# Kernel tuning notes

Measured on AMD Instinct MI355X. Metric: run time of the kernel, lower is better.

The kernel has to match this reference:

```python
import jax, jax.numpy as jnp
import numpy as np

FILTER_SIZE = 1024
NUM_HEADS = 16
D_HEAD = FILTER_SIZE // NUM_HEADS
LN_EPS = 1e-5


def setup_inputs() -> dict:
    key = jax.random.key(0)
    ks = jax.random.split(key, 10)
    B, T, D = 2, 2048, FILTER_SIZE
    s = 1.0 / np.sqrt(D)
    return {
        "x": jax.random.normal(ks[0], (B, T, D), dtype=jnp.float32),
        "Wq": jax.random.normal(ks[1], (D, D), dtype=jnp.float32) * s,
        "bq": jnp.zeros((D,), dtype=jnp.float32),
        "Wk": jax.random.normal(ks[2], (D, D), dtype=jnp.float32) * s,
        "bk": jnp.zeros((D,), dtype=jnp.float32),
        "Wv": jax.random.normal(ks[3], (D, D), dtype=jnp.float32) * s,
        "bv": jnp.zeros((D,), dtype=jnp.float32),
        "Wo": jax.random.normal(ks[4], (D, D), dtype=jnp.float32) * s,
        "bo": jnp.zeros((D,), dtype=jnp.float32),
        "gamma": jnp.ones((D,), dtype=jnp.float32),
        "beta": jnp.zeros((D,), dtype=jnp.float32),
    }


def reference(x, Wq, bq, Wk, bk, Wv, bv, Wo, bo, gamma, beta):
    B, T, D = x.shape
    H, Dh = NUM_HEADS, D_HEAD
    # Note: source splits features as (d_head, heads) with heads LAST.
    q = (x @ Wq.T + bq).reshape(B, T, Dh, H)
    k = (x @ Wk.T + bk).reshape(B, T, Dh, H)
    v = (x @ Wv.T + bv).reshape(B, T, Dh, H)
    scale = 1.0 / np.sqrt(Dh).astype(np.float32)
    # scores: (B, H, T, T)
    scores = jnp.einsum("bidh,bjdh->bhij", q, k) * scale
    attn = jax.nn.softmax(scores, axis=-1)  # dropout is identity in eval
    out = jnp.einsum("bhij,bjdh->bidh", attn, v)  # (B, T, Dh, H)
    out = out.reshape(B, T, D)  # matches permute(0,2,3,1).reshape in torch
    out = out @ Wo.T + bo
    out = out + x
    mu = jnp.mean(out, axis=-1, keepdims=True)
    var = jnp.var(out, axis=-1, keepdims=True)
    out = (out - mu) * jax.lax.rsqrt(var + LN_EPS) * gamma + beta
    return out
```

## Files before the change

### kernel.cpp

```cpp
#include <hip/hip_runtime.h>
#include <stdint.h>

#define T_SEQ 2048
#define D_MODEL 1024
#define NH 16
#define DH 64
#define NROWS 4096

typedef __bf16 bf16x8 __attribute__((ext_vector_type(8)));
typedef float floatx4 __attribute__((ext_vector_type(4)));
typedef short short4v __attribute__((ext_vector_type(4)));
typedef short short8v __attribute__((ext_vector_type(8)));

#define AS1 __attribute__((address_space(1)))
#define AS3 __attribute__((address_space(3)))

static __device__ __forceinline__ void gl2lds16(const unsigned short* g, unsigned short* s) {
    __builtin_amdgcn_global_load_lds((const AS1 unsigned int*)g, (AS3 unsigned int*)s, 16, 0, 0);
}

static __device__ __forceinline__ unsigned short f32_bf16(float f) {
    union { float f; unsigned int u; } c; c.f = f;
    unsigned int u = c.u;
    u = u + 0x7FFFu + ((u >> 16) & 1u);
    return (unsigned short)(u >> 16);
}

static __device__ __forceinline__ unsigned int pack2_bf16(float a, float b) {
    return (unsigned int)f32_bf16(a) | ((unsigned int)f32_bf16(b) << 16);
}

static __device__ __forceinline__ floatx4 mfma16(bf16x8 a, bf16x8 b, floatx4 c) {
    return __builtin_amdgcn_mfma_f32_16x16x32_bf16(a, b, c, 0, 0, 0);
}

static __device__ __forceinline__ floatx4 mfma16k16(short4v a, short4v b, floatx4 c) {
#if defined(__HIP_DEVICE_COMPILE__)
    return __builtin_amdgcn_mfma_f32_16x16x16bf16_1k(a, b, c, 0, 0, 0);
#else
    (void)a; (void)b;
    return c;
#endif
}

#define QSCALE 0.1803368801111204f
#define EXP2_SHIFT 10.0f
#define WAITCNT_VM(n) (0x0F70 | (n))

__global__ __launch_bounds__(256) void k_conv_all(const float* __restrict__ x,
                                                  const float* __restrict__ Wq,
                                                  const float* __restrict__ Wk,
                                                  const float* __restrict__ Wv,
                                                  const float* __restrict__ Wo,
                                                  unsigned short* __restrict__ x_bf,
                                                  unsigned short* __restrict__ wqkv_bf,
                                                  unsigned short* __restrict__ wo_bf) {
    int b = blockIdx.x, t = threadIdx.x;
    if (b < 4096) {
        int i = b * 1024 + t * 4;
        float4 v = *(const float4*)(x + i);
        uint2 o;
        o.x = pack2_bf16(v.x, v.y);
        o.y = pack2_bf16(v.z, v.w);
        *(uint2*)(x_bf + i) = o;
    } else if (b < 7168) {
        int idx = b - 4096;
        int tensor = idx >> 10, np = idx & 1023;
        const float* src = tensor == 0 ? Wq : tensor == 1 ? Wk : Wv;
        int f = (np & 63) * 16 + (np >> 6);
        int c = t * 4;
        float4 v = *(const float4*)(src + (long)f * D_MODEL + c);
        uint2 o;
        o.x = pack2_bf16(v.x, v.y);
        o.y = pack2_bf16(v.z, v.w);
        *(uint2*)(wqkv_bf + ((long)tensor * D_MODEL + np) * D_MODEL + c) = o;
    } else {
        int n = b - 7168;
        int fp = t * 4;
        const float* row = Wo + (long)n * D_MODEL;
        unsigned short o[4];
        #pragma unroll
        for (int k = 0; k < 4; k++) {
            int f = fp + k;
            o[k] = f32_bf16(row[(f & 63) * 16 + (f >> 6)]);
        }
        *(uint2*)(wo_bf + (long)n * D_MODEL + fp) = *(const uint2*)o;
    }
}

template <int BN, int MODE>
__global__ __launch_bounds__(256) void k_gemm(const unsigned short* __restrict__ A,
                                              const unsigned short* __restrict__ W,
                                              const float* __restrict__ b0,
                                              const float* __restrict__ b1,
                                              const float* __restrict__ b2,
                                              const float* __restrict__ resid,
                                              unsigned short* __restrict__ out_bf,
                                              unsigned short* __restrict__ vtg,
                                              float* __restrict__ out_f32) {
    constexpr int NT = BN / 32;
    constexpr int NCB = BN / 32;
    constexpr int NDMA = 4 + NCB;
    __shared__ unsigned short lds_a[2 * 128 * 64];
    __shared__ unsigned short lds_b[2 * BN * 64];
    const int tid = threadIdx.x;
    const int w = tid >> 6, l = tid & 63;
    const int lrow = l & 15, lq = l >> 4;
    const int wm = (w >> 1) * 64, wn = (w & 1) * (BN / 2);
    const int L = blockIdx.x;
    const int bx = (L & 7) * 4 + ((L >> 3) & 3);
    const int by = L >> 5;
    const long am0 = (long)bx * 128;
    const long wn0 = (long)by * BN;

    floatx4 acc[4][NT] = {};
    const int grow = l >> 3;
    const int gcol = ((l & 7) ^ grow) * 8;
    const int sw8 = (lrow & 7);

    auto stage = [&](int ki, int sel) {
        unsigned short* la = lds_a + sel * 8192;
        unsigned short* lb = lds_b + sel * (BN * 64);
        int k0 = ki * 64;
        #pragma unroll
        for (int c = 0; c < 4; c++) {
            int chunk = w * 4 + c;
            gl2lds16(A + (am0 + chunk * 8 + grow) * D_MODEL + k0 + gcol, la + chunk * 512);
        }
        #pragma unroll
        for (int c = 0; c < NCB; c++) {
            int chunk = w * NCB + c;
            gl2lds16(W + (wn0 + chunk * 8 + grow) * D_MODEL + k0 + gcol, lb + chunk * 512);
        }
    };

    stage(0, 0);

    for (int i = 0; i < 16; i++) {
        const int cur = i & 1;
        if (i < 15) {
            stage(i + 1, 1 - cur);
            __builtin_amdgcn_s_waitcnt(WAITCNT_VM(NDMA));
        } else {
            __builtin_amdgcn_s_waitcnt(WAITCNT_VM(0));
        }
        __builtin_amdgcn_s_barrier();

        const unsigned short* la = lds_a + cur * 8192;
        const unsigned short* lb = lds_b + cur * (BN * 64);
        bf16x8 af[4][2], bf[NT][2];
        #pragma unroll
        for (int mt = 0; mt < 4; mt++)
            #pragma unroll
            for (int ks = 0; ks < 2; ks++)
                af[mt][ks] = *(const bf16x8*)(la + (wm + mt * 16 + lrow) * 64 +
                                              (((ks * 4 + lq) ^ sw8) * 8));
        #pragma unroll
        for (int nt = 0; nt < NT; nt++)
            #pragma unroll
            for (int ks = 0; ks < 2; ks++)
                bf[nt][ks] = *(const bf16x8*)(lb + (wn + nt * 16 + lrow) * 64 +
                                              (((ks * 4 + lq) ^ sw8) * 8));
        #pragma unroll
        for (int mt = 0; mt < 4; mt++)
            #pragma unroll
            for (int nt = 0; nt < NT; nt++)
                #pragma unroll
                for (int ks = 0; ks < 2; ks++)
                    acc[mt][nt] = mfma16(af[mt][ks], bf[nt][ks], acc[mt][nt]);
        __builtin_amdgcn_s_barrier();
    }

    if (MODE == 0) {
        int tensor = by >> 3;
        int nbase = (by & 7) * 128;
        const float* bias = tensor == 0 ? b0 : tensor == 1 ? b1 : b2;
        float scale = tensor == 0 ? QSCALE : 1.0f;
        if (tensor < 2) {
            unsigned short* outt = out_bf + (size_t)tensor * (32u * T_SEQ * DH);
            #pragma unroll
            for (int mt = 0; mt < 4; mt++) {
                #pragma unroll
                for (int nt = 0; nt < NT; nt++) {
                    int n = nbase + wn + nt * 16 + lrow;
                    int h = n >> 6, d = n & 63;
                    float bb = bias[d * 16 + h];
                    #pragma unroll
                    for (int r = 0; r < 4; r++) {
                        int row = (int)am0 + wm + mt * 16 + lq * 4 + r;
                        float v = (acc[mt][nt][r] + bb) * scale;
                        int b = row >> 11, i = row & 2047;
                        long idx = ((long)(b * 16 + h) * T_SEQ + i) * DH + d;
                        outt[idx] = f32_bf16(v);
                    }
                }
            }
        } else {
            int row0 = (int)am0 + wm;
            int b = row0 >> 11;
            int blk = (row0 & 2047) >> 6;
            #pragma unroll
            for (int nt = 0; nt < NT; nt++) {
                int n = nbase + wn + nt * 16 + lrow;
                int h = n >> 6, d = n & 63;
                float bb = bias[d * 16 + h];
                long base = (((long)(b * 16 + h) * 64 + d) * 32 + blk) * 64;
                #pragma unroll
                for (int mt = 0; mt < 4; mt++) {
                    uint2 o;
                    o.x = pack2_bf16(acc[mt][nt][0] + bb, acc[mt][nt][1] + bb);
                    o.y = pack2_bf16(acc[mt][nt][2] + bb, acc[mt][nt][3] + bb);
                    *(uint2*)(vtg + base + lq * 16 + mt * 4) = o;
                }
            }
        }
    } else {
        #pragma unroll
        for (int mt = 0; mt < 4; mt++) {
            #pragma unroll
            for (int nt = 0; nt < NT; nt++) {
                int n = (int)wn0 + wn + nt * 16 + lrow;
                float bb = b0[n];
                #pragma unroll
                for (int r = 0; r < 4; r++) {
                    int row = (int)am0 + wm + mt * 16 + lq * 4 + r;
                    long idx = (long)row * D_MODEL + n;
                    out_f32[idx] = acc[mt][nt][r] + bb + resid[idx];
                }
            }
        }
    }
}

__global__ __launch_bounds__(256) void k_attn(const unsigned short* __restrict__ q_ws,
                                              const unsigned short* __restrict__ k_ws,
                                              const unsigned short* __restrict__ vtg,
                                              unsigned short* __restrict__ att) {
    __shared__ unsigned short kbuf[2 * 64 * 64];
    __shared__ unsigned short vbuf[2 * 64 * 64];
    const int tid = threadIdx.x;
    const int w = tid >> 6, l = tid & 63;
    const int lrow = l & 15, lq = l >> 4;
    const int sw = lrow & 7;
    const int L = blockIdx.x;
    const int bh = (L & 7) * 4 + ((L >> 3) & 3);
    const int i0 = (L >> 5) * 128;
    const unsigned short* kh = k_ws + (long)bh * T_SEQ * DH;
    const unsigned short* vh = vtg + (long)bh * 64 * T_SEQ;

    const int rl = l >> 3;
    const int gl = ((l & 7) ^ rl) * 8;

    bf16x8 qf[2][2];
    #pragma unroll
    for (int qt = 0; qt < 2; qt++) {
        const unsigned short* qp =
            q_ws + ((long)bh * T_SEQ + i0 + w * 32 + qt * 16 + lrow) * DH + lq * 8;
        qf[qt][0] = *(const bf16x8*)qp;
        qf[qt][1] = *(const bf16x8*)(qp + 32);
    }
    floatx4 o_acc[2][4] = {};
    floatx4 l_acc[2] = {};
    const short4v ones = {0x3F80, 0x3F80, 0x3F80, 0x3F80};

    auto stage = [&](int jt, int sel) {
        unsigned short* kd = kbuf + sel * 4096 + (w * 2) * 512;
        unsigned short* vd = vbuf + sel * 4096 + (w * 2) * 512;
        #pragma unroll
        for (int c = 0; c < 2; c++) {
            int row = w * 16 + c * 8 + rl;
            gl2lds16(kh + ((long)(jt * 64 + row)) * 64 + gl, kd + c * 512);
            gl2lds16(vh + ((long)row * 32 + jt) * 64 + gl, vd + c * 512);
        }
    };

    stage(0, 0);

    constexpr int NTILE = T_SEQ / 64;
    for (int jt = 0; jt < NTILE; jt++) {
        const int cur = jt & 1;
        if (jt < NTILE - 1) {
            stage(jt + 1, 1 - cur);
            __builtin_amdgcn_s_waitcnt(WAITCNT_VM(4));
        } else {
            __builtin_amdgcn_s_waitcnt(WAITCNT_VM(0));
        }
        __builtin_amdgcn_s_barrier();

        const unsigned short* kb_ = kbuf + cur * 4096;
        const unsigned short* vb_ = vbuf + cur * 4096;

        floatx4 s0[4], s1[4];
        #pragma unroll
        for (int nt = 0; nt < 4; nt++) {
            const unsigned short* kp = kb_ + (nt * 16 + lrow) * 64;
            bf16x8 ka = *(const bf16x8*)(kp + ((lq ^ sw) * 8));
            bf16x8 kb = *(const bf16x8*)(kp + (((lq + 4) ^ sw) * 8));
            floatx4 c0 = {-EXP2_SHIFT, -EXP2_SHIFT, -EXP2_SHIFT, -EXP2_SHIFT};
            floatx4 c1 = c0;
            c0 = mfma16(ka, qf[0][0], c0);
            c0 = mfma16(kb, qf[0][1], c0);
            c1 = mfma16(ka, qf[1][0], c1);
            c1 = mfma16(kb, qf[1][1], c1);
            s0[nt] = c0;
            s1[nt] = c1;
        }
        short4v pf0[4], pf1[4];
        #pragma unroll
        for (int nt = 0; nt < 4; nt++) {
            {
                float p0 = __builtin_amdgcn_exp2f(s0[nt][0]);
                float p1 = __builtin_amdgcn_exp2f(s0[nt][1]);
                float p2 = __builtin_amdgcn_exp2f(s0[nt][2]);
                float p3 = __builtin_amdgcn_exp2f(s0[nt][3]);
                uint2 pk;
                pk.x = __builtin_amdgcn_perm(__float_as_uint(p1), __float_as_uint(p0), 0x07060302);
                pk.y = __builtin_amdgcn_perm(__float_as_uint(p3), __float_as_uint(p2), 0x07060302);
                union { uint2 u; short4v s4; } cv; cv.u = pk;
                pf0[nt] = cv.s4;
                l_acc[0] = mfma16k16(ones, pf0[nt], l_acc[0]);
            }
            {
                float p0 = __builtin_amdgcn_exp2f(s1[nt][0]);
                float p1 = __builtin_amdgcn_exp2f(s1[nt][1]);
                float p2 = __builtin_amdgcn_exp2f(s1[nt][2]);
                float p3 = __builtin_amdgcn_exp2f(s1[nt][3]);
                uint2 pk;
                pk.x = __builtin_amdgcn_perm(__float_as_uint(p1), __float_as_uint(p0), 0x07060302);
                pk.y = __builtin_amdgcn_perm(__float_as_uint(p3), __float_as_uint(p2), 0x07060302);
                union { uint2 u; short4v s4; } cv; cv.u = pk;
                pf1[nt] = cv.s4;
                l_acc[1] = mfma16k16(ones, pf1[nt], l_acc[1]);
            }
        }
        #pragma unroll
        for (int dt = 0; dt < 4; dt++) {
            const unsigned short* vp = vb_ + (dt * 16 + lrow) * 64;
            short8v v01 = *(const short8v*)(vp + (((2 * lq) ^ sw) * 8));
            short8v v23 = *(const short8v*)(vp + (((2 * lq + 1) ^ sw) * 8));
            short4v va = __builtin_shufflevector(v01, v01, 0, 1, 2, 3);
            short4v vb = __builtin_shufflevector(v01, v01, 4, 5, 6, 7);
            short4v vc = __builtin_shufflevector(v23, v23, 0, 1, 2, 3);
            short4v vd = __builtin_shufflevector(v23, v23, 4, 5, 6, 7);
            o_acc[0][dt] = mfma16k16(va, pf0[0], o_acc[0][dt]);
            o_acc[0][dt] = mfma16k16(vb, pf0[1], o_acc[0][dt]);
            o_acc[0][dt] = mfma16k16(vc, pf0[2], o_acc[0][dt]);
            o_acc[0][dt] = mfma16k16(vd, pf0[3], o_acc[0][dt]);
            o_acc[1][dt] = mfma16k16(va, pf1[0], o_acc[1][dt]);
            o_acc[1][dt] = mfma16k16(vb, pf1[1], o_acc[1][dt]);
            o_acc[1][dt] = mfma16k16(vc, pf1[2], o_acc[1][dt]);
            o_acc[1][dt] = mfma16k16(vd, pf1[3], o_acc[1][dt]);
        }
        __builtin_amdgcn_s_barrier();
    }
    int h = bh & 15, b = bh >> 4;
    #pragma unroll
    for (int qt = 0; qt < 2; qt++) {
        float rl2 = 1.0f / l_acc[qt][0];
        int i = i0 + w * 32 + qt * 16 + lrow;
        unsigned short* orow = att + ((long)(b * T_SEQ + i)) * D_MODEL + h * 64;
        #pragma unroll
        for (int dt = 0; dt < 4; dt++) {
            uint2 o;
            o.x = pack2_bf16(o_acc[qt][dt][0] * rl2, o_acc[qt][dt][1] * rl2);
            o.y = pack2_bf16(o_acc[qt][dt][2] * rl2, o_acc[qt][dt][3] * rl2);
            *(uint2*)(orow + dt * 16 + lq * 4) = o;
        }
    }
}

__global__ __launch_bounds__(256) void k_ln(float* __restrict__ io,
                                            const float* __restrict__ gamma,
                                            const float* __restrict__ beta) {
    int row = blockIdx.x, t = threadIdx.x;
    float* p = io + (long)row * D_MODEL + t * 4;
    float4 v = *(float4*)p;
    float s = v.x + v.y + v.z + v.w;
    float ss = v.x * v.x + v.y * v.y + v.z * v.z + v.w * v.w;
    #pragma unroll
    for (int m = 1; m < 64; m <<= 1) {
        s += __shfl_xor(s, m);
        ss += __shfl_xor(ss, m);
    }
    __shared__ float red[8];
    if ((t & 63) == 0) { red[t >> 6] = s; red[4 + (t >> 6)] = ss; }
    __syncthreads();
    s = red[0] + red[1] + red[2] + red[3];
    ss = red[4] + red[5] + red[6] + red[7];
    float mu = s * (1.0f / 1024.0f);
    float var = ss * (1.0f / 1024.0f) - mu * mu;
    float rstd = rsqrtf(var + 1e-5f);
    float4 g = *(const float4*)(gamma + t * 4);
    float4 be = *(const float4*)(beta + t * 4);
    float4 o;
    o.x = (v.x - mu) * rstd * g.x + be.x;
    o.y = (v.y - mu) * rstd * g.y + be.y;
    o.z = (v.z - mu) * rstd * g.z + be.z;
    o.w = (v.w - mu) * rstd * g.w + be.w;
    *(float4*)p = o;
}

extern "C" void kernel_launch(void* const* d_in, const int* in_sizes, int n_in,
                              void* d_out, int out_size, void* d_ws, size_t ws_size,
                              hipStream_t stream) {
    const float* x = (const float*)d_in[0];
    const float* Wq = (const float*)d_in[1];
    const float* bq = (const float*)d_in[2];
    const float* Wk = (const float*)d_in[3];
    const float* bk = (const float*)d_in[4];
    const float* Wv = (const float*)d_in[5];
    const float* bv = (const float*)d_in[6];
    const float* Wo = (const float*)d_in[7];
    const float* bo = (const float*)d_in[8];
    const float* gamma = (const float*)d_in[9];
    const float* beta = (const float*)d_in[10];
    float* out = (float*)d_out;

    char* ws = (char*)d_ws;
    unsigned short* x_bf = (unsigned short*)(ws);
    unsigned short* wqkv_bf = (unsigned short*)(ws + ((size_t)8 << 20));
    unsigned short* wo_bf = (unsigned short*)(ws + ((size_t)14 << 20));
    unsigned short* qkv_ws = (unsigned short*)(ws + ((size_t)16 << 20));
    unsigned short* att = x_bf;

    unsigned short* q_ws = qkv_ws;
    unsigned short* k_ws = qkv_ws + (size_t)32 * T_SEQ * DH;
    unsigned short* vtg = qkv_ws + (size_t)64 * T_SEQ * DH;

    k_conv_all<<<8192, 256, 0, stream>>>(x, Wq, Wk, Wv, Wo, x_bf, wqkv_bf, wo_bf);

    k_gemm<128, 0><<<768, 256, 0, stream>>>(
        x_bf, wqkv_bf, bq, bk, bv, nullptr, qkv_ws, vtg, nullptr);

    k_attn<<<512, 256, 0, stream>>>(q_ws, k_ws, vtg, att);

    k_gemm<64, 1><<<512, 256, 0, stream>>>(
        att, wo_bf, bo, nullptr, nullptr, x, nullptr, nullptr, out);

    k_ln<<<NROWS, 256, 0, stream>>>(out, gamma, beta);
}
```

Baseline: 212.7 us.

## Use K=32 MFMA for PV by round-tripping P through LDS and plain V^T layout

The attention PV product moves from 16x16x16 bf16 MFMAs on register fragments to 16x16x32 MFMAs. P is written to a per-wave LDS buffer and read back in the K=32 operand layout. V^T is now stored as a plain [bh][d][T] array instead of blocked 64-wide tiles, and the staging loads are adjusted to match. This halves the MFMA instruction count for PV and the row-sum, at the cost of extra LDS writes and reads for P plus 8KB more shared memory per block.

New measurement: 214.3 us. No clear change (+0.7%).

```diff
diff --git a/kernel.cpp b/kernel.cpp
--- a/kernel.cpp
+++ b/kernel.cpp
@@ -9,8 +9,6 @@
 
 typedef __bf16 bf16x8 __attribute__((ext_vector_type(8)));
 typedef float floatx4 __attribute__((ext_vector_type(4)));
-typedef short short4v __attribute__((ext_vector_type(4)));
-typedef short short8v __attribute__((ext_vector_type(8)));
 
 #define AS1 __attribute__((address_space(1)))
 #define AS3 __attribute__((address_space(3)))
@@ -32,15 +30,6 @@
 
 static __device__ __forceinline__ floatx4 mfma16(bf16x8 a, bf16x8 b, floatx4 c) {
     return __builtin_amdgcn_mfma_f32_16x16x32_bf16(a, b, c, 0, 0, 0);
-}
-
-static __device__ __forceinline__ floatx4 mfma16k16(short4v a, short4v b, floatx4 c) {
-#if defined(__HIP_DEVICE_COMPILE__)
-    return __builtin_amdgcn_mfma_f32_16x16x16bf16_1k(a, b, c, 0, 0, 0);
-#else
-    (void)a; (void)b;
-    return c;
-#endif
 }
 
 #define QSCALE 0.1803368801111204f
@@ -96,7 +85,7 @@
                                               const float* __restrict__ b2,
                                               const float* __restrict__ resid,
                                               unsigned short* __restrict__ out_bf,
-                                              unsigned short* __restrict__ vtg,
+                                              unsigned short* __restrict__ vt,
                                               float* __restrict__ out_f32) {
     constexpr int NT = BN / 32;
     constexpr int NCB = BN / 32;
@@ -198,19 +187,19 @@
         } else {
             int row0 = (int)am0 + wm;
             int b = row0 >> 11;
-            int blk = (row0 & 2047) >> 6;
+            int j0 = row0 & 2047;
             #pragma unroll
             for (int nt = 0; nt < NT; nt++) {
                 int n = nbase + wn + nt * 16 + lrow;
                 int h = n >> 6, d = n & 63;
                 float bb = bias[d * 16 + h];
-                long base = (((long)(b * 16 + h) * 64 + d) * 32 + blk) * 64;
+                long base = ((long)(b * 16 + h) * 64 + d) * T_SEQ;
                 #pragma unroll
                 for (int mt = 0; mt < 4; mt++) {
                     uint2 o;
                     o.x = pack2_bf16(acc[mt][nt][0] + bb, acc[mt][nt][1] + bb);
                     o.y = pack2_bf16(acc[mt][nt][2] + bb, acc[mt][nt][3] + bb);
-                    *(uint2*)(vtg + base + lq * 16 + mt * 4) = o;
+                    *(uint2*)(vt + base + j0 + mt * 16 + lq * 4) = o;
                 }
             }
         }
@@ -234,10 +223,11 @@
 
 __global__ __launch_bounds__(256) void k_attn(const unsigned short* __restrict__ q_ws,
                                               const unsigned short* __restrict__ k_ws,
-                                              const unsigned short* __restrict__ vtg,
+                                              const unsigned short* __restrict__ vt,
                                               unsigned short* __restrict__ att) {
     __shared__ unsigned short kbuf[2 * 64 * 64];
     __shared__ unsigned short vbuf[2 * 64 * 64];
+    __shared__ unsigned short pbuf[4][16 * 64];
     const int tid = threadIdx.x;
     const int w = tid >> 6, l = tid & 63;
     const int lrow = l & 15, lq = l >> 4;
@@ -246,7 +236,7 @@
     const int bh = (L & 7) * 4 + ((L >> 3) & 3);
     const int i0 = (L >> 5) * 128;
     const unsigned short* kh = k_ws + (long)bh * T_SEQ * DH;
-    const unsigned short* vh = vtg + (long)bh * 64 * T_SEQ;
+    const unsigned short* vh = vt + (long)bh * 64 * T_SEQ;
 
     const int rl = l >> 3;
     const int gl = ((l & 7) ^ rl) * 8;
@@ -261,7 +251,22 @@
     }
     floatx4 o_acc[2][4] = {};
     floatx4 l_acc[2] = {};
-    const short4v ones = {0x3F80, 0x3F80, 0x3F80, 0x3F80};
+    bf16x8 ones;
+    {
+        union { unsigned short s[8]; bf16x8 v; } cv;
+        #pragma unroll
+        for (int k = 0; k < 8; k++) cv.s[k] = 0x3F80;
+        ones = cv.v;
+    }
+
+    unsigned short* pw = &pbuf[w][0];
+    int pwr[4], prd[2];
+    #pragma unroll
+    for (int nt = 0; nt < 4; nt++)
+        pwr[nt] = lrow * 64 + (((nt * 2 + (lq >> 1)) ^ sw) * 8) + (lq & 1) * 4;
+    #pragma unroll
+    for (int h = 0; h < 2; h++)
+        prd[h] = lrow * 64 + (((h * 4 + lq) ^ sw) * 8);
 
     auto stage = [&](int jt, int sel) {
         unsigned short* kd = kbuf + sel * 4096 + (w * 2) * 512;
@@ -270,7 +275,7 @@
         for (int c = 0; c < 2; c++) {
             int row = w * 16 + c * 8 + rl;
             gl2lds16(kh + ((long)(jt * 64 + row)) * 64 + gl, kd + c * 512);
-            gl2lds16(vh + ((long)row * 32 + jt) * 64 + gl, vd + c * 512);
+            gl2lds16(vh + (long)row * T_SEQ + jt * 64 + gl, vd + c * 512);
         }
     };
 
@@ -305,51 +310,36 @@
             s0[nt] = c0;
             s1[nt] = c1;
         }
-        short4v pf0[4], pf1[4];
-        #pragma unroll
-        for (int nt = 0; nt < 4; nt++) {
-            {
-                float p0 = __builtin_amdgcn_exp2f(s0[nt][0]);
-                float p1 = __builtin_amdgcn_exp2f(s0[nt][1]);
-                float p2 = __builtin_amdgcn_exp2f(s0[nt][2]);
-                float p3 = __builtin_amdgcn_exp2f(s0[nt][3]);
+        bf16x8 vf[4][2];
+        #pragma unroll
+        for (int dt = 0; dt < 4; dt++) {
+            const unsigned short* vp = vb_ + (dt * 16 + lrow) * 64;
+            vf[dt][0] = *(const bf16x8*)(vp + ((lq ^ sw) * 8));
+            vf[dt][1] = *(const bf16x8*)(vp + (((lq + 4) ^ sw) * 8));
+        }
+        #pragma unroll
+        for (int qt = 0; qt < 2; qt++) {
+            const floatx4* s = (qt == 0) ? s0 : s1;
+            #pragma unroll
+            for (int nt = 0; nt < 4; nt++) {
+                float p0 = __builtin_amdgcn_exp2f(s[nt][0]);
+                float p1 = __builtin_amdgcn_exp2f(s[nt][1]);
+                float p2 = __builtin_amdgcn_exp2f(s[nt][2]);
+                float p3 = __builtin_amdgcn_exp2f(s[nt][3]);
                 uint2 pk;
                 pk.x = __builtin_amdgcn_perm(__float_as_uint(p1), __float_as_uint(p0), 0x07060302);
                 pk.y = __builtin_amdgcn_perm(__float_as_uint(p3), __float_as_uint(p2), 0x07060302);
-                union { uint2 u; short4v s4; } cv; cv.u = pk;
-                pf0[nt] = cv.s4;
-                l_acc[0] = mfma16k16(ones, pf0[nt], l_acc[0]);
+                *(uint2*)(pw + pwr[nt]) = pk;
             }
-            {
-                float p0 = __builtin_amdgcn_exp2f(s1[nt][0]);
-                float p1 = __builtin_amdgcn_exp2f(s1[nt][1]);
-                float p2 = __builtin_amdgcn_exp2f(s1[nt][2]);
-                float p3 = __builtin_amdgcn_exp2f(s1[nt][3]);
-                uint2 pk;
-                pk.x = __builtin_amdgcn_perm(__float_as_uint(p1), __float_as_uint(p0), 0x07060302);
-                pk.y = __builtin_amdgcn_perm(__float_as_uint(p3), __float_as_uint(p2), 0x07060302);
-                union { uint2 u; short4v s4; } cv; cv.u = pk;
-                pf1[nt] = cv.s4;
-                l_acc[1] = mfma16k16(ones, pf1[nt], l_acc[1]);
+            bf16x8 pf0 = *(const bf16x8*)(pw + prd[0]);
+            bf16x8 pf1 = *(const bf16x8*)(pw + prd[1]);
+            l_acc[qt] = mfma16(ones, pf0, l_acc[qt]);
+            l_acc[qt] = mfma16(ones, pf1, l_acc[qt]);
+            #pragma unroll
+            for (int dt = 0; dt < 4; dt++) {
+                o_acc[qt][dt] = mfma16(vf[dt][0], pf0, o_acc[qt][dt]);
+                o_acc[qt][dt] = mfma16(vf[dt][1], pf1, o_acc[qt][dt]);
             }
-        }
-        #pragma unroll
-        for (int dt = 0; dt < 4; dt++) {
-            const unsigned short* vp = vb_ + (dt * 16 + lrow) * 64;
-            short8v v01 = *(const short8v*)(vp + (((2 * lq) ^ sw) * 8));
-            short8v v23 = *(const short8v*)(vp + (((2 * lq + 1) ^ sw) * 8));
-            short4v va = __builtin_shufflevector(v01, v01, 0, 1, 2, 3);
-            short4v vb = __builtin_shufflevector(v01, v01, 4, 5, 6, 7);
-            short4v vc = __builtin_shufflevector(v23, v23, 0, 1, 2, 3);
-            short4v vd = __builtin_shufflevector(v23, v23, 4, 5, 6, 7);
-            o_acc[0][dt] = mfma16k16(va, pf0[0], o_acc[0][dt]);
-            o_acc[0][dt] = mfma16k16(vb, pf0[1], o_acc[0][dt]);
-            o_acc[0][dt] = mfma16k16(vc, pf0[2], o_acc[0][dt]);
-            o_acc[0][dt] = mfma16k16(vd, pf0[3], o_acc[0][dt]);
-            o_acc[1][dt] = mfma16k16(va, pf1[0], o_acc[1][dt]);
-            o_acc[1][dt] = mfma16k16(vb, pf1[1], o_acc[1][dt]);
-            o_acc[1][dt] = mfma16k16(vc, pf1[2], o_acc[1][dt]);
-            o_acc[1][dt] = mfma16k16(vd, pf1[3], o_acc[1][dt]);
         }
         __builtin_amdgcn_s_barrier();
     }
@@ -425,14 +415,14 @@
 
     unsigned short* q_ws = qkv_ws;
     unsigned short* k_ws = qkv_ws + (size_t)32 * T_SEQ * DH;
-    unsigned short* vtg = qkv_ws + (size_t)64 * T_SEQ * DH;
+    unsigned short* vt = qkv_ws + (size_t)64 * T_SEQ * DH;
 
     k_conv_all<<<8192, 256, 0, stream>>>(x, Wq, Wk, Wv, Wo, x_bf, wqkv_bf, wo_bf);
 
     k_gemm<128, 0><<<768, 256, 0, stream>>>(
-        x_bf, wqkv_bf, bq, bk, bv, nullptr, qkv_ws, vtg, nullptr);
-
-    k_attn<<<512, 256, 0, stream>>>(q_ws, k_ws, vtg, att);
+        x_bf, wqkv_bf, bq, bk, bv, nullptr, qkv_ws, vt, nullptr);
+
+    k_attn<<<512, 256, 0, stream>>>(q_ws, k_ws, vt, att);
 
     k_gemm<64, 1><<<512, 256, 0, stream>>>(
         att, wo_bf, bo, nullptr, nullptr, x, nullptr, nullptr, out);
```
